# Kernel tuning notes

Measured on AMD Instinct MI355X. Metric: run time of the kernel, lower is better.

Reference implementation:

```python
import jax, jax.numpy as jnp
import numpy as np

N = 50000        # nodes
E = 1600000      # edges
NDIM_IN = 64
HID = 128        # hardcoded hidden width of first SAGELayer in E-GraphSAGE
NDIM_OUT = 128
EDIM = 32
EMBEDIM = 128
NCLASS = 2       # bin=True


def setup_inputs() -> dict:
    key = jax.random.key(0)
    ks = jax.random.split(key, 12)
    g = lambda k, shape: jax.random.normal(k, shape, jnp.float32) / np.sqrt(np.float32(shape[0]))
    return {
        "nfeats": jax.random.normal(ks[0], (N, NDIM_IN), jnp.float32),
        "efeats": jax.random.normal(ks[1], (E, EDIM), jnp.float32),
        "src": jax.random.randint(ks[2], (E,), 0, N),
        "dst": jax.random.randint(ks[3], (E,), 0, N),
        # SAGE layer 1: W_msg [ndim_in+edim -> 128], W_apply [ndim_in+128 -> 128]
        "Wm1": g(ks[4], (NDIM_IN + EDIM, HID)), "bm1": jnp.zeros((HID,), jnp.float32),
        "Wa1": g(ks[5], (NDIM_IN + HID, HID)), "ba1": jnp.zeros((HID,), jnp.float32),
        # SAGE layer 2: W_msg [128+edim -> ndim_out], W_apply [128+ndim_out -> ndim_out]
        "Wm2": g(ks[6], (HID + EDIM, NDIM_OUT)), "bm2": jnp.zeros((NDIM_OUT,), jnp.float32),
        "Wa2": g(ks[7], (HID + NDIM_OUT, NDIM_OUT)), "ba2": jnp.zeros((NDIM_OUT,), jnp.float32),
        # MLPPredictorEmbed: [2*ndim_out -> embedim] -> relu -> [embedim -> 2]
        "W1": g(ks[8], (2 * NDIM_OUT, EMBEDIM)), "b1": jnp.zeros((EMBEDIM,), jnp.float32),
        "W2": g(ks[9], (EMBEDIM, NCLASS)), "b2": jnp.zeros((NCLASS,), jnp.float32),
    }


def _sage_layer(h, efeats, src, dst, Wm, bm, Wa, ba):
    # per-edge message: relu(W_msg([h_src || e]))  -> [E, dout]
    m = jax.nn.relu(jnp.concatenate([h[src], efeats], axis=-1) @ Wm + bm)
    # mean aggregation by destination node (0 for isolated nodes, like DGL fn.mean)
    s = jax.ops.segment_sum(m, dst, num_segments=N)
    cnt = jax.ops.segment_sum(jnp.ones((m.shape[0], 1), m.dtype), dst, num_segments=N)
    h_neigh = s / jnp.maximum(cnt, 1.0)
    # node update: relu(W_apply([h || h_neigh]))
    return jax.nn.relu(jnp.concatenate([h, h_neigh], axis=-1) @ Wa + ba)


def reference(nfeats, efeats, src, dst,
              Wm1, bm1, Wa1, ba1, Wm2, bm2, Wa2, ba2,
              W1, b1, W2, b2):
    h = _sage_layer(nfeats, efeats, src, dst, Wm1, bm1, Wa1, ba1)   # [N, 128]
    h = _sage_layer(h, efeats, src, dst, Wm2, bm2, Wa2, ba2)        # [N, ndim_out]
    # edge predictor: MLP on [h_u || h_v] per edge
    z = jnp.concatenate([h[src], h[dst]], axis=-1)                   # [E, 2*ndim_out]
    score = jax.nn.relu(z @ W1 + b1) @ W2 + b2                       # [E, 2]
    return score
```

## Files before the change

### kernel.cpp

```cpp
#include <hip/hip_runtime.h>

#define N_NODES 50000
#define N_EDGES 1600000

typedef _Float16 h8 __attribute__((ext_vector_type(8)));
typedef float f4 __attribute__((ext_vector_type(4)));

__device__ inline h8 ld_h8(const _Float16* p) { return *(const h8*)p; }

__device__ inline h8 cvt2h8(f4 a, f4 b) {
    h8 r;
    r[0] = (_Float16)a[0]; r[1] = (_Float16)a[1]; r[2] = (_Float16)a[2]; r[3] = (_Float16)a[3];
    r[4] = (_Float16)b[0]; r[5] = (_Float16)b[1]; r[6] = (_Float16)b[2]; r[7] = (_Float16)b[3];
    return r;
}


__global__ void prep_weights(const float* __restrict__ Wm1, const float* __restrict__ Wa1,
                             const float* __restrict__ Wm2, const float* __restrict__ Wa2,
                             const float* __restrict__ W1,
                             _Float16* __restrict__ Wm1t, _Float16* __restrict__ Wa1t,
                             _Float16* __restrict__ Wm2t, _Float16* __restrict__ Wa2t,
                             _Float16* __restrict__ W1t)
{
    int i = blockIdx.x * 256 + threadIdx.x;
    if (i < 12288) {
        int o = i / 96, k = i % 96;
        int ks = k >> 5, q = (k >> 3) & 3, j = k & 7;
        int c = q ^ ((o >> 1) & 3);
        Wm1t[(ks * 128 + o) * 32 + c * 8 + j] = (_Float16)Wm1[k * 128 + o];
    } else if (i < 36864) {
        int jj = i - 12288; int o = jj / 192, k = jj % 192;
        Wa1t[o * 200 + k] = (_Float16)Wa1[k * 128 + o];
    } else if (i < 57344) {
        int jj = i - 36864; int o = jj / 160, k = jj % 160;
        int ks = k >> 5, q = (k >> 3) & 3, j = k & 7;
        int c = q ^ ((o >> 1) & 3);
        Wm2t[(ks * 128 + o) * 32 + c * 8 + j] = (_Float16)Wm2[k * 128 + o];
    } else if (i < 90112) {
        int jj = i - 57344; int o = jj >> 8, k = jj & 255;
        Wa2t[(o << 8) + k] = (_Float16)Wa2[k * 128 + o];
    } else if (i < 122880) {
        int jj = i - 90112; int o = jj >> 8, k = jj & 255;
        W1t[(o << 8) + k] = (_Float16)W1[k * 128 + o];
    }
}

__global__ void cvt_nfeats(const float* __restrict__ nf, _Float16* __restrict__ nf16)
{
    int i = blockIdx.x * 256 + threadIdx.x;
    nf16[i] = (_Float16)nf[i];
}


__global__ void hist_kernel(const int* __restrict__ dst, int* __restrict__ cnt)
{
    int e = blockIdx.x * 256 + threadIdx.x;
    atomicAdd(cnt + dst[e], 1);
}

__global__ void scan1_kernel(const int* __restrict__ cnt, int* __restrict__ tmp,
                             int* __restrict__ bsum)
{
    __shared__ int sh[256];
    int t = threadIdx.x, i = blockIdx.x * 256 + t;
    int v = (i < N_NODES) ? cnt[i] : 0;
    sh[t] = v; __syncthreads();
    for (int off = 1; off < 256; off <<= 1) {
        int x = (t >= off) ? sh[t - off] : 0;
        __syncthreads();
        sh[t] += x;
        __syncthreads();
    }
    if (i < N_NODES) tmp[i] = sh[t];
    if (t == 255) bsum[blockIdx.x] = sh[255];
}

__global__ void scan2_kernel(const int* __restrict__ bsum, int* __restrict__ bbase)
{
    __shared__ int sh[256];
    int t = threadIdx.x;
    int v = (t < 196) ? bsum[t] : 0;
    sh[t] = v; __syncthreads();
    for (int off = 1; off < 256; off <<= 1) {
        int x = (t >= off) ? sh[t - off] : 0;
        __syncthreads();
        sh[t] += x;
        __syncthreads();
    }
    if (t < 196) bbase[t] = sh[t] - v;
}

__global__ void scan3_kernel(const int* __restrict__ cnt, const int* __restrict__ tmp,
                             const int* __restrict__ bbase, int* __restrict__ cursor)
{
    int t = threadIdx.x, b = blockIdx.x, i = b * 256 + t;
    if (i < N_NODES) cursor[i] = tmp[i] - cnt[i] + bbase[b];
}

__global__ void scatter_kernel(const int* __restrict__ src, const int* __restrict__ dst,
                               int* __restrict__ cursor,
                               int2* __restrict__ pairs, int* __restrict__ dsts)
{
    int e = blockIdx.x * 256 + threadIdx.x;
    int d = dst[e];
    int pos = atomicAdd(cursor + d, 1);
    pairs[pos] = make_int2(e, src[e]);
    dsts[pos] = d;
}

template<int KSRC_H, int MINW>
__launch_bounds__(256, MINW)
__global__ void msg_kernel_sorted(const _Float16* __restrict__ ntab,
                                  const float* __restrict__ efeats,
                                  const int2* __restrict__ pairs,
                                  const int* __restrict__ dsts,
                                  const _Float16* __restrict__ Wt,
                                  const float* __restrict__ bias,
                                  float* __restrict__ sacc)
{
    constexpr int EFSTEP = KSRC_H / 32;
    constexpr int KSTEPS = EFSTEP + 1;
    constexpr int BH = (KSRC_H + 32) * 128;
    constexpr int BBYTES = BH * 2;
    constexpr int SCRBYTES = 4 * 16 * 132 * 4;
    constexpr int LDSBYTES = BBYTES > SCRBYTES ? BBYTES : SCRBYTES;
    __shared__ __align__(16) char smem[LDSBYTES];
    _Float16* Bsh = (_Float16*)smem;

    const int tid = threadIdx.x;
    const int wave = tid >> 6, lane = tid & 63;
    const int q = lane >> 4, l15 = lane & 15;
    const int wbase = blockIdx.x * 128 + wave * 32;

    const int2 p0 = pairs[wbase + l15];
    const int2 p1 = pairs[wbase + 16 + l15];
    const _Float16* r0 = ntab + (size_t)p0.y * KSRC_H + q * 8;
    const _Float16* r1 = ntab + (size_t)p1.y * KSRC_H + q * 8;
    h8 a0p = ld_h8(r0);
    h8 a1p = ld_h8(r1);
    const float* ep0 = efeats + (size_t)p0.x * 32 + q * 8;
    const float* ep1 = efeats + (size_t)p1.x * 32 + q * 8;
    f4 e0a, e0b, e1a, e1b;
    if constexpr (KSRC_H > 64) {
        e0a = *(const f4*)ep0; e0b = *(const f4*)(ep0 + 4);
        e1a = *(const f4*)ep1; e1b = *(const f4*)(ep1 + 4);
    }

    {
        const uint4* s4 = (const uint4*)Wt;
        uint4* d4 = (uint4*)smem;
        constexpr int n4 = BH / 8;
        for (int i = tid; i < n4; i += 256) d4[i] = s4[i];
    }
    __syncthreads();

    f4 acc[2][8];
#pragma unroll
    for (int t = 0; t < 2; t++)
#pragma unroll
        for (int nt = 0; nt < 8; nt++) acc[t][nt] = (f4){0.f, 0.f, 0.f, 0.f};

    const _Float16* bp = Bsh + l15 * 32 + ((q ^ ((l15 >> 1) & 3)) << 3);
#pragma unroll
    for (int ks = 0; ks < KSTEPS; ks++) {
        h8 a0, a1;
        if (ks == 0) {
            a0 = a0p; a1 = a1p;
        } else if (ks < EFSTEP) {
            a0 = ld_h8(r0 + ks * 32);
            a1 = ld_h8(r1 + ks * 32);
        } else {
            if constexpr (KSRC_H > 64) {
                a0 = cvt2h8(e0a, e0b);
                a1 = cvt2h8(e1a, e1b);
            } else {
                a0 = cvt2h8(*(const f4*)ep0, *(const f4*)(ep0 + 4));
                a1 = cvt2h8(*(const f4*)ep1, *(const f4*)(ep1 + 4));
            }
        }
#pragma unroll
        for (int nt = 0; nt < 8; nt++) {
            h8 b = ld_h8(bp + ks * 4096 + nt * 512);
            acc[0][nt] = __builtin_amdgcn_mfma_f32_16x16x32_f16(a0, b, acc[0][nt], 0, 0, 0);
            acc[1][nt] = __builtin_amdgcn_mfma_f32_16x16x32_f16(a1, b, acc[1][nt], 0, 0, 0);
        }
    }

    __syncthreads();

    float* wsch = (float*)smem + wave * 2112;

    float bv[8];
#pragma unroll
    for (int nt = 0; nt < 8; nt++) bv[nt] = bias[nt * 16 + l15];

    const int4 dv0 = *(const int4*)(dsts + wbase + q * 4);
    const int4 dv1 = *(const int4*)(dsts + wbase + 16 + q * 4);
    const int df0 = __shfl(dv0.x, l15, 64);
    const int dl0 = __shfl(dv0.w, 48 + l15, 64);
    const int df1 = __shfl(dv1.x, l15, 64);
    const int dl1 = __shfl(dv1.w, 48 + l15, 64);

    auto reduce16 = [&](const f4 (&a)[8], int df, int dl, int rbase) {
        if (df == dl) {
            float sv[8];
#pragma unroll
            for (int nt = 0; nt < 8; nt++) {
                float s = fmaxf(a[nt][0] + bv[nt], 0.f) + fmaxf(a[nt][1] + bv[nt], 0.f)
                        + fmaxf(a[nt][2] + bv[nt], 0.f) + fmaxf(a[nt][3] + bv[nt], 0.f);
                s += __shfl_xor(s, 16, 64);
                s += __shfl_xor(s, 32, 64);
                sv[nt] = s;
            }
#pragma unroll
            for (int i = 0; i < 2; i++) {
                float x = (q == 0) ? sv[i*4] : (q == 1) ? sv[i*4+1] : (q == 2) ? sv[i*4+2] : sv[i*4+3];
                atomicAdd(sacc + (size_t)df * 128 + i * 64 + lane, x);
            }
        } else {
#pragma unroll
            for (int nt = 0; nt < 8; nt++)
#pragma unroll
                for (int r = 0; r < 4; r++)
                    wsch[(q * 4 + r) * 132 + nt * 16 + l15] = fmaxf(a[nt][r] + bv[nt], 0.f);
            const int rb = __builtin_amdgcn_readfirstlane(rbase);
            float s0 = 0.f, s1 = 0.f;
            int dp = dsts[rb];
            for (int rr = 0; rr < 16; rr++) {
                const int d = dsts[rb + rr];
                const float v0 = wsch[rr * 132 + lane];
                const float v1 = wsch[rr * 132 + 64 + lane];
                if (d != dp) {
                    atomicAdd(sacc + (size_t)dp * 128 + lane, s0);
                    atomicAdd(sacc + (size_t)dp * 128 + 64 + lane, s1);
                    s0 = v0; s1 = v1; dp = d;
                } else {
                    s0 += v0; s1 += v1;
                }
            }
            atomicAdd(sacc + (size_t)dp * 128 + lane, s0);
            atomicAdd(sacc + (size_t)dp * 128 + 64 + lane, s1);
        }
    };

    if (df0 == dl1) {
        float sv[8];
#pragma unroll
        for (int nt = 0; nt < 8; nt++) {
            float s = fmaxf(acc[0][nt][0] + bv[nt], 0.f) + fmaxf(acc[0][nt][1] + bv[nt], 0.f)
                    + fmaxf(acc[0][nt][2] + bv[nt], 0.f) + fmaxf(acc[0][nt][3] + bv[nt], 0.f)
                    + fmaxf(acc[1][nt][0] + bv[nt], 0.f) + fmaxf(acc[1][nt][1] + bv[nt], 0.f)
                    + fmaxf(acc[1][nt][2] + bv[nt], 0.f) + fmaxf(acc[1][nt][3] + bv[nt], 0.f);
            s += __shfl_xor(s, 16, 64);
            s += __shfl_xor(s, 32, 64);
            sv[nt] = s;
        }
#pragma unroll
        for (int i = 0; i < 2; i++) {
            float x = (q == 0) ? sv[i*4] : (q == 1) ? sv[i*4+1] : (q == 2) ? sv[i*4+2] : sv[i*4+3];
            atomicAdd(sacc + (size_t)df0 * 128 + i * 64 + lane, x);
        }
    } else {
        reduce16(acc[0], df0, dl0, wbase);
        reduce16(acc[1], df1, dl1, wbase + 16);
    }
}

template<int KSRC_H, bool SWIZ, int KPAD>
__launch_bounds__(256)
__global__ void apply_kernel(const _Float16* __restrict__ ntab,
                             const float* __restrict__ sacc,
                             const int* __restrict__ cnt,
                             const _Float16* __restrict__ Wt,
                             const float* __restrict__ bias,
                             _Float16* __restrict__ outtab)
{
    constexpr int KSTEPS = (KSRC_H + 128) / 32;
    __shared__ __align__(16) _Float16 Bsh[128 * KPAD];

    const int tid = threadIdx.x;
    if (SWIZ) {
        const uint4* s4 = (const uint4*)Wt;
        uint4* d4 = (uint4*)Bsh;
        for (int i = tid; i < 4096; i += 256) {
            int n = i >> 5, c = i & 31;
            d4[(n << 5) | (c ^ (n & 31))] = s4[i];
        }
    } else {
        const uint4* s4 = (const uint4*)Wt;
        uint4* d4 = (uint4*)Bsh;
        constexpr int n4 = 128 * KPAD / 8;
        for (int i = tid; i < n4; i += 256) d4[i] = s4[i];
    }
    __syncthreads();

    const int wave = tid >> 6, lane = tid & 63;
    const int q = lane >> 4, l15 = lane & 15;
    const int nbase = blockIdx.x * 128 + wave * 32;

    const int n0 = nbase + l15, n1 = nbase + 16 + l15;
    const int n0c = min(n0, N_NODES - 1), n1c = min(n1, N_NODES - 1);
    const _Float16* r0 = ntab + (size_t)n0c * KSRC_H;
    const _Float16* r1 = ntab + (size_t)n1c * KSRC_H;
    const float rcp0 = 1.0f / fmaxf((float)cnt[n0c], 1.0f);
    const float rcp1 = 1.0f / fmaxf((float)cnt[n1c], 1.0f);

    f4 acc[2][8];
#pragma unroll
    for (int t = 0; t < 2; t++)
#pragma unroll
        for (int nt = 0; nt < 8; nt++) acc[t][nt] = (f4){0.f, 0.f, 0.f, 0.f};

#pragma unroll
    for (int ks = 0; ks < KSTEPS; ks++) {
        h8 a0, a1;
        if (ks < KSRC_H / 32) {
            a0 = ld_h8(r0 + ks * 32 + q * 8);
            a1 = ld_h8(r1 + ks * 32 + q * 8);
        } else {
            const int kk = ks * 32 - KSRC_H + q * 8;
            const float* p0 = sacc + (size_t)n0c * 128 + kk;
            const float* p1 = sacc + (size_t)n1c * 128 + kk;
            f4 u0 = *(const f4*)p0 * rcp0, v0 = *(const f4*)(p0 + 4) * rcp0;
            f4 u1 = *(const f4*)p1 * rcp1, v1 = *(const f4*)(p1 + 4) * rcp1;
            a0 = cvt2h8(u0, v0);
            a1 = cvt2h8(u1, v1);
        }
#pragma unroll
        for (int nt = 0; nt < 8; nt++) {
            h8 b;
            if (SWIZ) {
                const int nrow = nt * 16 + l15;
                const int chunk = ((ks << 2) | q) ^ (nrow & 31);
                b = ld_h8(Bsh + (((nrow << 5) | chunk) << 3));
            } else {
                b = ld_h8(&Bsh[(nt * 16 + l15) * KPAD + ks * 32 + q * 8]);
            }
            acc[0][nt] = __builtin_amdgcn_mfma_f32_16x16x32_f16(a0, b, acc[0][nt], 0, 0, 0);
            acc[1][nt] = __builtin_amdgcn_mfma_f32_16x16x32_f16(a1, b, acc[1][nt], 0, 0, 0);
        }
    }

#pragma unroll
    for (int nt = 0; nt < 8; nt++) {
        const int col = nt * 16 + l15;
        const float bv = bias[col];
#pragma unroll
        for (int t = 0; t < 2; t++)
#pragma unroll
            for (int r = 0; r < 4; r++) {
                const int node = nbase + t * 16 + q * 4 + r;
                if (node < N_NODES) {
                    float v = fmaxf(acc[t][nt][r] + bv, 0.f);
                    outtab[(size_t)node * 128 + col] = (_Float16)v;
                }
            }
    }
}

__launch_bounds__(256)
__global__ void node_pq_kernel(const _Float16* __restrict__ h2,
                               const _Float16* __restrict__ W1t,
                               const float* __restrict__ b1,
                               _Float16* __restrict__ P,
                               float* __restrict__ Q)
{
    __shared__ __align__(16) _Float16 Bsh[128 * 256];

    const int tid = threadIdx.x;
    {
        const uint4* s4 = (const uint4*)W1t;
        uint4* d4 = (uint4*)Bsh;
        for (int i = tid; i < 4096; i += 256) {
            int n = i >> 5, c = i & 31;
            d4[(n << 5) | (c ^ (n & 31))] = s4[i];
        }
    }
    __syncthreads();

    const int wave = tid >> 6, lane = tid & 63;
    const int q = lane >> 4, l15 = lane & 15;
    const int nbase = blockIdx.x * 128 + wave * 32;

    const int n0 = nbase + l15, n1 = nbase + 16 + l15;
    const int n0c = min(n0, N_NODES - 1), n1c = min(n1, N_NODES - 1);
    const _Float16* r0 = h2 + (size_t)n0c * 128;
    const _Float16* r1 = h2 + (size_t)n1c * 128;

    f4 accP[2][8], accQ[2][8];
#pragma unroll
    for (int t = 0; t < 2; t++)
#pragma unroll
        for (int nt = 0; nt < 8; nt++) {
            accP[t][nt] = (f4){0.f, 0.f, 0.f, 0.f};
            accQ[t][nt] = (f4){0.f, 0.f, 0.f, 0.f};
        }

#pragma unroll
    for (int ks = 0; ks < 4; ks++) {
        h8 a0 = ld_h8(r0 + ks * 32 + q * 8);
        h8 a1 = ld_h8(r1 + ks * 32 + q * 8);
#pragma unroll
        for (int nt = 0; nt < 8; nt++) {
            const int nrow = nt * 16 + l15;
            const int cP = ((ks << 2) | q) ^ (nrow & 31);
            h8 bP = ld_h8(Bsh + (((nrow << 5) | cP) << 3));
            accP[0][nt] = __builtin_amdgcn_mfma_f32_16x16x32_f16(a0, bP, accP[0][nt], 0, 0, 0);
            accP[1][nt] = __builtin_amdgcn_mfma_f32_16x16x32_f16(a1, bP, accP[1][nt], 0, 0, 0);
            const int cQ = (((ks + 4) << 2) | q) ^ (nrow & 31);
            h8 bQ = ld_h8(Bsh + (((nrow << 5) | cQ) << 3));
            accQ[0][nt] = __builtin_amdgcn_mfma_f32_16x16x32_f16(a0, bQ, accQ[0][nt], 0, 0, 0);
            accQ[1][nt] = __builtin_amdgcn_mfma_f32_16x16x32_f16(a1, bQ, accQ[1][nt], 0, 0, 0);
        }
    }

#pragma unroll
    for (int nt = 0; nt < 8; nt++) {
        const int col = nt * 16 + l15;
        const float bq = b1[col];
#pragma unroll
        for (int t = 0; t < 2; t++)
#pragma unroll
            for (int r = 0; r < 4; r++) {
                const int node = nbase + t * 16 + q * 4 + r;
                if (node < N_NODES) {
                    P[(size_t)node * 128 + col] = (_Float16)accP[t][nt][r];
                    Q[(size_t)node * 128 + col] = accQ[t][nt][r] + bq;
                }
            }
    }
}

__launch_bounds__(256, 4)
__global__ void pred_elem_kernel(const _Float16* __restrict__ P,
                                 const float* __restrict__ Q,
                                 const int2* __restrict__ pairs,
                                 const int* __restrict__ dsts,
                                 const float* __restrict__ W2,
                                 const float* __restrict__ b2,
                                 float* __restrict__ out)
{
    __shared__ __align__(16) float w20sh[128];
    __shared__ __align__(16) float w21sh[128];

    const int tid = threadIdx.x;
    if (tid < 128) {
        w20sh[tid] = W2[tid * 2 + 0];
        w21sh[tid] = W2[tid * 2 + 1];
    }
    __syncthreads();

    const int slot = blockIdx.x * 256 + tid;
    const int2 pr = pairs[slot];
    const int d = dsts[slot];
    const _Float16* prow = P + (size_t)pr.y * 128;
    const float* qrow = Q + (size_t)d * 128;

    float o0 = 0.f, o1 = 0.f;
#pragma unroll
    for (int c = 0; c < 4; c++) {
        h8 pv[4];
#pragma unroll
        for (int i = 0; i < 4; i++) pv[i] = ld_h8(prow + c * 32 + i * 8);
        f4 qv[8];
#pragma unroll
        for (int i = 0; i < 8; i++) qv[i] = *(const f4*)(qrow + c * 32 + i * 4);
#pragma unroll
        for (int i = 0; i < 8; i++) {
            const f4 w0 = *(const f4*)(w20sh + c * 32 + i * 4);
            const f4 w1 = *(const f4*)(w21sh + c * 32 + i * 4);
#pragma unroll
            for (int j = 0; j < 4; j++) {
                const float pvf = (float)pv[i >> 1][(i & 1) * 4 + j];
                const float y = fmaxf(pvf + qv[i][j], 0.f);
                o0 += y * w0[j];
                o1 += y * w1[j];
            }
        }
    }

    out[(size_t)pr.x * 2 + 0] = o0 + b2[0];
    out[(size_t)pr.x * 2 + 1] = o1 + b2[1];
}

__launch_bounds__(256)
__global__ void pred_kernel(const _Float16* __restrict__ h2,
                            const int* __restrict__ src,
                            const int* __restrict__ dst,
                            const _Float16* __restrict__ W1t,
                            const float* __restrict__ b1,
                            const float* __restrict__ W2,
                            const float* __restrict__ b2,
                            float* __restrict__ out)
{
    __shared__ __align__(16) _Float16 Bsh[128 * 256];

    const int tid = threadIdx.x;
    {
        const uint4* s4 = (const uint4*)W1t;
        uint4* d4 = (uint4*)Bsh;
        for (int i = tid; i < 4096; i += 256) {
            int n = i >> 5, c = i & 31;
            d4[(n << 5) | (c ^ (n & 31))] = s4[i];
        }
    }
    __syncthreads();

    const int wave = tid >> 6, lane = tid & 63;
    const int q = lane >> 4, l15 = lane & 15;
    const int ebase = blockIdx.x * 128 + wave * 32;

    const int e0 = ebase + l15, e1 = ebase + 16 + l15;
    const _Float16* rs0 = h2 + (size_t)src[e0] * 128;
    const _Float16* rd0 = h2 + (size_t)dst[e0] * 128;
    const _Float16* rs1 = h2 + (size_t)src[e1] * 128;
    const _Float16* rd1 = h2 + (size_t)dst[e1] * 128;

    f4 acc[2][8];
#pragma unroll
    for (int t = 0; t < 2; t++)
#pragma unroll
        for (int nt = 0; nt < 8; nt++) acc[t][nt] = (f4){0.f, 0.f, 0.f, 0.f};

#pragma unroll
    for (int ks = 0; ks < 8; ks++) {
        h8 a0, a1;
        if (ks < 4) {
            a0 = ld_h8(rs0 + ks * 32 + q * 8);
            a1 = ld_h8(rs1 + ks * 32 + q * 8);
        } else {
            a0 = ld_h8(rd0 + (ks - 4) * 32 + q * 8);
            a1 = ld_h8(rd1 + (ks - 4) * 32 + q * 8);
        }
#pragma unroll
        for (int nt = 0; nt < 8; nt++) {
            const int nrow = nt * 16 + l15;
            const int chunk = ((ks << 2) | q) ^ (nrow & 31);
            h8 b = ld_h8(Bsh + (((nrow << 5) | chunk) << 3));
            acc[0][nt] = __builtin_amdgcn_mfma_f32_16x16x32_f16(a0, b, acc[0][nt], 0, 0, 0);
            acc[1][nt] = __builtin_amdgcn_mfma_f32_16x16x32_f16(a1, b, acc[1][nt], 0, 0, 0);
        }
    }

    float o[2][4][2];
#pragma unroll
    for (int t = 0; t < 2; t++)
#pragma unroll
        for (int r = 0; r < 4; r++) { o[t][r][0] = 0.f; o[t][r][1] = 0.f; }

#pragma unroll
    for (int nt = 0; nt < 8; nt++) {
        const int nrow = nt * 16 + l15;
        const float bv = b1[nrow];
        const float w20 = W2[nrow * 2 + 0];
        const float w21 = W2[nrow * 2 + 1];
#pragma unroll
        for (int t = 0; t < 2; t++)
#pragma unroll
            for (int r = 0; r < 4; r++) {
                float y = fmaxf(acc[t][nt][r] + bv, 0.f);
                o[t][r][0] += y * w20;
                o[t][r][1] += y * w21;
            }
    }

#pragma unroll
    for (int m = 1; m < 16; m <<= 1) {
#pragma unroll
        for (int t = 0; t < 2; t++)
#pragma unroll
            for (int r = 0; r < 4; r++) {
                o[t][r][0] += __shfl_xor(o[t][r][0], m, 64);
                o[t][r][1] += __shfl_xor(o[t][r][1], m, 64);
            }
    }

    if (l15 < 8) {
        const int r = l15 >> 1, c = l15 & 1;
        const float bb = c ? b2[1] : b2[0];
#pragma unroll
        for (int t = 0; t < 2; t++) {
            float v0 = (r == 0) ? o[t][0][0] : (r == 1) ? o[t][1][0] : (r == 2) ? o[t][2][0] : o[t][3][0];
            float v1 = (r == 0) ? o[t][0][1] : (r == 1) ? o[t][1][1] : (r == 2) ? o[t][2][1] : o[t][3][1];
            float v = (c ? v1 : v0) + bb;
            out[(size_t)(ebase + t * 16 + q * 4 + r) * 2 + c] = v;
        }
    }
}


extern "C" void kernel_launch(void* const* d_in, const int* in_sizes, int n_in,
                              void* d_out, int out_size, void* d_ws, size_t ws_size,
                              hipStream_t stream)
{
    const float* nfeats = (const float*)d_in[0];
    const float* efeats = (const float*)d_in[1];
    const int*   src    = (const int*)d_in[2];
    const int*   dst    = (const int*)d_in[3];
    const float* Wm1 = (const float*)d_in[4],  *bm1 = (const float*)d_in[5];
    const float* Wa1 = (const float*)d_in[6],  *ba1 = (const float*)d_in[7];
    const float* Wm2 = (const float*)d_in[8],  *bm2 = (const float*)d_in[9];
    const float* Wa2 = (const float*)d_in[10], *ba2 = (const float*)d_in[11];
    const float* W1  = (const float*)d_in[12], *b1  = (const float*)d_in[13];
    const float* W2  = (const float*)d_in[14], *b2  = (const float*)d_in[15];
    float* out = (float*)d_out;

    char* ws = (char*)d_ws;
    float*     s     = (float*)(ws);
    int*       cnt   = (int*)(ws + 25600000);
    int*       tmp   = (int*)(ws + 25800000);
    int*       cursor= (int*)(ws + 26000000);
    int*       bsum  = (int*)(ws + 26200000);
    int*       bbase = (int*)(ws + 26201024);
    _Float16*  nf16  = (_Float16*)(ws + 26202048);
    int2*      pairs = (int2*)(ws + 32602048);
    int*       dsts  = (int*)(ws + 45402048);
    _Float16*  h1    = (_Float16*)(ws + 51802048);
    _Float16*  Wm1t  = (_Float16*)(ws + 64602048);
    _Float16*  Wa1t  = (_Float16*)(ws + 64626624);
    _Float16*  Wm2t  = (_Float16*)(ws + 64677824);
    _Float16*  Wa2t  = (_Float16*)(ws + 64718784);
    _Float16*  W1t   = (_Float16*)(ws + 64784320);

    const bool big_ws = ws_size >= (size_t)77800000;
    _Float16* h2 = big_ws ? (_Float16*)(ws + 64849920)
                          : (_Float16*)(ws + 26202048);

    hipMemsetAsync(s, 0, 25600000, stream);
    hipMemsetAsync(cnt, 0, 200000, stream);

    prep_weights<<<480, 256, 0, stream>>>(Wm1, Wa1, Wm2, Wa2, W1, Wm1t, Wa1t, Wm2t, Wa2t, W1t);
    cvt_nfeats<<<12500, 256, 0, stream>>>(nfeats, nf16);

    hist_kernel<<<6250, 256, 0, stream>>>(dst, cnt);
    scan1_kernel<<<196, 256, 0, stream>>>(cnt, tmp, bsum);
    scan2_kernel<<<1, 256, 0, stream>>>(bsum, bbase);
    scan3_kernel<<<196, 256, 0, stream>>>(cnt, tmp, bbase, cursor);
    scatter_kernel<<<6250, 256, 0, stream>>>(src, dst, cursor, pairs, dsts);

    msg_kernel_sorted<64, 5><<<12500, 256, 0, stream>>>(nf16, efeats, pairs, dsts, Wm1t, bm1, s);
    apply_kernel<64, false, 200><<<391, 256, 0, stream>>>(nf16, s, cnt, Wa1t, ba1, h1);

    hipMemsetAsync(s, 0, 25600000, stream);
    msg_kernel_sorted<128, 4><<<12500, 256, 0, stream>>>(h1, efeats, pairs, dsts, Wm2t, bm2, s);
    apply_kernel<128, true, 256><<<391, 256, 0, stream>>>(h1, s, cnt, Wa2t, ba2, h2);

    if (big_ws) {
        _Float16* P = h1;
        float*    Q = s;
        node_pq_kernel<<<391, 256, 0, stream>>>(h2, W1t, b1, P, Q);
        pred_elem_kernel<<<6250, 256, 0, stream>>>(P, Q, pairs, dsts, W2, b2, out);
    } else {
        pred_kernel<<<12500, 256, 0, stream>>>(h2, src, dst, W1t, b1, W2, b2, out);
    }
}
```

Measured before the change: 1.021 ms.

## Pre-sort edge features to fp16 in scatter and hoist gathers in message kernel

The scatter kernel now also writes edge features converted to fp16 in sorted-edge order, so both message kernels read them contiguously at half the bytes instead of gathering fp32 rows by edge id. The message kernel issues all neighbour-row and edge-feature loads, destination ids and bias up front, before the weight copy into shared memory. The mixed-destination reduction now halves its scratch space, takes destination ids from registers through shuffles instead of reloading them from global memory, and checks each 16-row half separately. This costs a larger workspace (used only when it is big enough) and an extra fp16 write pass in scatter, and it lowers the layer-1 occupancy hint from 5 to 4.

Result: no change. 1.027 ms (+0.6%).

```diff
diff --git a/kernel.cpp b/kernel.cpp
--- a/kernel.cpp
+++ b/kernel.cpp
@@ -109,10 +109,34 @@
     dsts[pos] = d;
 }
 
-template<int KSRC_H, int MINW>
+__global__ void scatter_kernel_ef(const int* __restrict__ src, const int* __restrict__ dst,
+                                  const float* __restrict__ efeats,
+                                  int* __restrict__ cursor,
+                                  int2* __restrict__ pairs, int* __restrict__ dsts,
+                                  _Float16* __restrict__ efs)
+{
+    int e = blockIdx.x * 256 + threadIdx.x;
+    int d = dst[e];
+    const float* er = efeats + (size_t)e * 32;
+    f4 v0 = *(const f4*)(er + 0),  v1 = *(const f4*)(er + 4);
+    f4 v2 = *(const f4*)(er + 8),  v3 = *(const f4*)(er + 12);
+    f4 v4 = *(const f4*)(er + 16), v5 = *(const f4*)(er + 20);
+    f4 v6 = *(const f4*)(er + 24), v7 = *(const f4*)(er + 28);
+    int pos = atomicAdd(cursor + d, 1);
+    pairs[pos] = make_int2(e, src[e]);
+    dsts[pos] = d;
+    _Float16* ew = efs + (size_t)pos * 32;
+    *(h8*)(ew + 0)  = cvt2h8(v0, v1);
+    *(h8*)(ew + 8)  = cvt2h8(v2, v3);
+    *(h8*)(ew + 16) = cvt2h8(v4, v5);
+    *(h8*)(ew + 24) = cvt2h8(v6, v7);
+}
+
+template<int KSRC_H, int MINW, bool EF16>
 __launch_bounds__(256, MINW)
 __global__ void msg_kernel_sorted(const _Float16* __restrict__ ntab,
                                   const float* __restrict__ efeats,
+                                  const _Float16* __restrict__ efs,
                                   const int2* __restrict__ pairs,
                                   const int* __restrict__ dsts,
                                   const _Float16* __restrict__ Wt,
@@ -123,7 +147,7 @@
     constexpr int KSTEPS = EFSTEP + 1;
     constexpr int BH = (KSRC_H + 32) * 128;
     constexpr int BBYTES = BH * 2;
-    constexpr int SCRBYTES = 4 * 16 * 132 * 4;
+    constexpr int SCRBYTES = 4 * 8 * 132 * 4;
     constexpr int LDSBYTES = BBYTES > SCRBYTES ? BBYTES : SCRBYTES;
     __shared__ __align__(16) char smem[LDSBYTES];
     _Float16* Bsh = (_Float16*)smem;
@@ -135,14 +159,28 @@
 
     const int2 p0 = pairs[wbase + l15];
     const int2 p1 = pairs[wbase + 16 + l15];
+    const int4 dv0 = *(const int4*)(dsts + wbase + q * 4);
+    const int4 dv1 = *(const int4*)(dsts + wbase + 16 + q * 4);
+    float bv[8];
+#pragma unroll
+    for (int nt = 0; nt < 8; nt++) bv[nt] = bias[nt * 16 + l15];
+
     const _Float16* r0 = ntab + (size_t)p0.y * KSRC_H + q * 8;
     const _Float16* r1 = ntab + (size_t)p1.y * KSRC_H + q * 8;
-    h8 a0p = ld_h8(r0);
-    h8 a1p = ld_h8(r1);
-    const float* ep0 = efeats + (size_t)p0.x * 32 + q * 8;
-    const float* ep1 = efeats + (size_t)p1.x * 32 + q * 8;
+    h8 aA[EFSTEP], aB[EFSTEP];
+#pragma unroll
+    for (int ks = 0; ks < EFSTEP; ks++) {
+        aA[ks] = ld_h8(r0 + ks * 32);
+        aB[ks] = ld_h8(r1 + ks * 32);
+    }
+    h8 ef0h, ef1h;
     f4 e0a, e0b, e1a, e1b;
-    if constexpr (KSRC_H > 64) {
+    if constexpr (EF16) {
+        ef0h = ld_h8(efs + (size_t)(wbase + l15) * 32 + q * 8);
+        ef1h = ld_h8(efs + (size_t)(wbase + 16 + l15) * 32 + q * 8);
+    } else {
+        const float* ep0 = efeats + (size_t)p0.x * 32 + q * 8;
+        const float* ep1 = efeats + (size_t)p1.x * 32 + q * 8;
         e0a = *(const f4*)ep0; e0b = *(const f4*)(ep0 + 4);
         e1a = *(const f4*)ep1; e1b = *(const f4*)(ep1 + 4);
     }
@@ -165,19 +203,11 @@
 #pragma unroll
     for (int ks = 0; ks < KSTEPS; ks++) {
         h8 a0, a1;
-        if (ks == 0) {
-            a0 = a0p; a1 = a1p;
-        } else if (ks < EFSTEP) {
-            a0 = ld_h8(r0 + ks * 32);
-            a1 = ld_h8(r1 + ks * 32);
+        if (ks < EFSTEP) {
+            a0 = aA[ks]; a1 = aB[ks];
         } else {
-            if constexpr (KSRC_H > 64) {
-                a0 = cvt2h8(e0a, e0b);
-                a1 = cvt2h8(e1a, e1b);
-            } else {
-                a0 = cvt2h8(*(const f4*)ep0, *(const f4*)(ep0 + 4));
-                a1 = cvt2h8(*(const f4*)ep1, *(const f4*)(ep1 + 4));
-            }
+            if constexpr (EF16) { a0 = ef0h; a1 = ef1h; }
+            else { a0 = cvt2h8(e0a, e0b); a1 = cvt2h8(e1a, e1b); }
         }
 #pragma unroll
         for (int nt = 0; nt < 8; nt++) {
@@ -189,46 +219,53 @@
 
     __syncthreads();
 
-    float* wsch = (float*)smem + wave * 2112;
-
-    float bv[8];
-#pragma unroll
-    for (int nt = 0; nt < 8; nt++) bv[nt] = bias[nt * 16 + l15];
-
-    const int4 dv0 = *(const int4*)(dsts + wbase + q * 4);
-    const int4 dv1 = *(const int4*)(dsts + wbase + 16 + q * 4);
-    const int df0 = __shfl(dv0.x, l15, 64);
-    const int dl0 = __shfl(dv0.w, 48 + l15, 64);
-    const int df1 = __shfl(dv1.x, l15, 64);
-    const int dl1 = __shfl(dv1.w, 48 + l15, 64);
-
-    auto reduce16 = [&](const f4 (&a)[8], int df, int dl, int rbase) {
-        if (df == dl) {
-            float sv[8];
-#pragma unroll
-            for (int nt = 0; nt < 8; nt++) {
-                float s = fmaxf(a[nt][0] + bv[nt], 0.f) + fmaxf(a[nt][1] + bv[nt], 0.f)
-                        + fmaxf(a[nt][2] + bv[nt], 0.f) + fmaxf(a[nt][3] + bv[nt], 0.f);
-                s += __shfl_xor(s, 16, 64);
-                s += __shfl_xor(s, 32, 64);
-                sv[nt] = s;
+    float* wsch = (float*)smem + wave * 1056;
+
+    const int df0 = __shfl(dv0.x, 0, 64);
+    const int dl0 = __shfl(dv0.w, 48, 64);
+    const int df1 = __shfl(dv1.x, 0, 64);
+    const int dl1 = __shfl(dv1.w, 48, 64);
+
+    auto unif16 = [&](const f4 (&a)[8], int d) {
+        float sv[8];
+#pragma unroll
+        for (int nt = 0; nt < 8; nt++) {
+            float s = fmaxf(a[nt][0] + bv[nt], 0.f) + fmaxf(a[nt][1] + bv[nt], 0.f)
+                    + fmaxf(a[nt][2] + bv[nt], 0.f) + fmaxf(a[nt][3] + bv[nt], 0.f);
+            s += __shfl_xor(s, 16, 64);
+            s += __shfl_xor(s, 32, 64);
+            sv[nt] = s;
+        }
+#pragma unroll
+        for (int i = 0; i < 2; i++) {
+            float x = (q == 0) ? sv[i*4] : (q == 1) ? sv[i*4+1] : (q == 2) ? sv[i*4+2] : sv[i*4+3];
+            atomicAdd(sacc + (size_t)d * 128 + i * 64 + lane, x);
+        }
+    };
+
+    auto scan16 = [&](const f4 (&a)[8], const int4 dv, int dfirst) {
+        int dp = dfirst;
+        float s0 = 0.f, s1 = 0.f;
+#pragma unroll
+        for (int h = 0; h < 2; h++) {
+            if ((q >> 1) == h) {
+                const int rloc = (q & 1) * 4;
+#pragma unroll
+                for (int nt = 0; nt < 8; nt++)
+#pragma unroll
+                    for (int r = 0; r < 4; r++)
+                        wsch[(rloc + r) * 132 + nt * 16 + l15] = fmaxf(a[nt][r] + bv[nt], 0.f);
             }
-#pragma unroll
-            for (int i = 0; i < 2; i++) {
-                float x = (q == 0) ? sv[i*4] : (q == 1) ? sv[i*4+1] : (q == 2) ? sv[i*4+2] : sv[i*4+3];
-                atomicAdd(sacc + (size_t)df * 128 + i * 64 + lane, x);
-            }
-        } else {
-#pragma unroll
-            for (int nt = 0; nt < 8; nt++)
-#pragma unroll
-                for (int r = 0; r < 4; r++)
-                    wsch[(q * 4 + r) * 132 + nt * 16 + l15] = fmaxf(a[nt][r] + bv[nt], 0.f);
-            const int rb = __builtin_amdgcn_readfirstlane(rbase);
-            float s0 = 0.f, s1 = 0.f;
-            int dp = dsts[rb];
-            for (int rr = 0; rr < 16; rr++) {
-                const int d = dsts[rb + rr];
+            asm volatile("s_waitcnt lgkmcnt(0)" ::: "memory");
+#pragma unroll
+            for (int rr = 0; rr < 8; rr++) {
+                const int rg = h * 8 + rr;
+                const int sl = (rg >> 2) << 4;
+                const int c = rg & 3;
+                const int d = (c == 0) ? __shfl(dv.x, sl, 64)
+                            : (c == 1) ? __shfl(dv.y, sl, 64)
+                            : (c == 2) ? __shfl(dv.z, sl, 64)
+                            :            __shfl(dv.w, sl, 64);
                 const float v0 = wsch[rr * 132 + lane];
                 const float v1 = wsch[rr * 132 + 64 + lane];
                 if (d != dp) {
@@ -239,9 +276,9 @@
                     s0 += v0; s1 += v1;
                 }
             }
-            atomicAdd(sacc + (size_t)dp * 128 + lane, s0);
-            atomicAdd(sacc + (size_t)dp * 128 + 64 + lane, s1);
-        }
+        }
+        atomicAdd(sacc + (size_t)dp * 128 + lane, s0);
+        atomicAdd(sacc + (size_t)dp * 128 + 64 + lane, s1);
     };
 
     if (df0 == dl1) {
@@ -262,8 +299,8 @@
             atomicAdd(sacc + (size_t)df0 * 128 + i * 64 + lane, x);
         }
     } else {
-        reduce16(acc[0], df0, dl0, wbase);
-        reduce16(acc[1], df1, dl1, wbase + 16);
+        if (df0 == dl0) unif16(acc[0], df0); else scan16(acc[0], dv0, df0);
+        if (df1 == dl1) unif16(acc[1], df1); else scan16(acc[1], dv1, df1);
     }
 }
 
@@ -623,9 +660,11 @@
     _Float16*  Wa2t  = (_Float16*)(ws + 64718784);
     _Float16*  W1t   = (_Float16*)(ws + 64784320);
 
-    const bool big_ws = ws_size >= (size_t)77800000;
+    const bool big_ws  = ws_size >= (size_t)77800000;
+    const bool ef16_ws = ws_size >= (size_t)180100000;
     _Float16* h2 = big_ws ? (_Float16*)(ws + 64849920)
                           : (_Float16*)(ws + 26202048);
+    _Float16* efs16 = (_Float16*)(ws + 77649920);
 
     hipMemsetAsync(s, 0, 25600000, stream);
     hipMemsetAsync(cnt, 0, 200000, stream);
@@ -637,13 +676,22 @@
     scan1_kernel<<<196, 256, 0, stream>>>(cnt, tmp, bsum);
     scan2_kernel<<<1, 256, 0, stream>>>(bsum, bbase);
     scan3_kernel<<<196, 256, 0, stream>>>(cnt, tmp, bbase, cursor);
-    scatter_kernel<<<6250, 256, 0, stream>>>(src, dst, cursor, pairs, dsts);
-
-    msg_kernel_sorted<64, 5><<<12500, 256, 0, stream>>>(nf16, efeats, pairs, dsts, Wm1t, bm1, s);
+    if (ef16_ws)
+        scatter_kernel_ef<<<6250, 256, 0, stream>>>(src, dst, efeats, cursor, pairs, dsts, efs16);
+    else
+        scatter_kernel<<<6250, 256, 0, stream>>>(src, dst, cursor, pairs, dsts);
+
+    if (ef16_ws)
+        msg_kernel_sorted<64, 4, true><<<12500, 256, 0, stream>>>(nf16, efeats, efs16, pairs, dsts, Wm1t, bm1, s);
+    else
+        msg_kernel_sorted<64, 4, false><<<12500, 256, 0, stream>>>(nf16, efeats, nullptr, pairs, dsts, Wm1t, bm1, s);
     apply_kernel<64, false, 200><<<391, 256, 0, stream>>>(nf16, s, cnt, Wa1t, ba1, h1);
 
     hipMemsetAsync(s, 0, 25600000, stream);
-    msg_kernel_sorted<128, 4><<<12500, 256, 0, stream>>>(h1, efeats, pairs, dsts, Wm2t, bm2, s);
+    if (ef16_ws)
+        msg_kernel_sorted<128, 4, true><<<12500, 256, 0, stream>>>(h1, efeats, efs16, pairs, dsts, Wm2t, bm2, s);
+    else
+        msg_kernel_sorted<128, 4, false><<<12500, 256, 0, stream>>>(h1, efeats, nullptr, pairs, dsts, Wm2t, bm2, s);
     apply_kernel<128, true, 256><<<391, 256, 0, stream>>>(h1, s, cnt, Wa2t, ba2, h2);
 
     if (big_ws) {
```
